# Kernel tuning notes

Measured on AMD Instinct MI355X. Metric: run time of the kernel, lower is better.

## Reference

```python
import jax, jax.numpy as jnp
import numpy as np

N_QUBITS = 6
N_LAYERS = 6
BATCH = 262144
DIM = 2 ** N_QUBITS  # 64 statevector amplitudes


def _apply_1q(s, U, q, n):
    # s: (M, 2^n) batch of statevectors, apply 2x2 gate U on wire q
    # (wire 0 = most significant bit, PennyLane convention)
    M = s.shape[0]
    st = s.reshape(M, 2 ** q, 2, 2 ** (n - 1 - q))
    out = jnp.einsum('ab,mxby->mxay', U, st)
    return out.reshape(M, 2 ** n)


def _apply_cnot(s, c, t, n):
    # CNOT(control=c, target=t): flip target bit where control bit == 1
    M = s.shape[0]
    a, b = (c, t) if c < t else (t, c)
    st = s.reshape(M, 2 ** a, 2, 2 ** (b - a - 1), 2, 2 ** (n - 1 - b))
    cax = 2 if c < t else 4
    tax = 4 if c < t else 2
    s0 = jnp.take(st, 0, axis=cax)
    s1 = jnp.take(st, 1, axis=cax)
    s1 = jnp.flip(s1, axis=tax - (1 if tax > cax else 0))
    out = jnp.stack([s0, s1], axis=cax)
    return out.reshape(M, 2 ** n)


def _rot(phi, theta, omega):
    # PennyLane Rot(phi, theta, omega) = RZ(omega) RY(theta) RZ(phi)
    c = jnp.cos(theta / 2).astype(jnp.complex64)
    s = jnp.sin(theta / 2).astype(jnp.complex64)
    ep = jnp.exp(-0.5j * (phi + omega).astype(jnp.complex64))
    em = jnp.exp(-0.5j * (phi - omega).astype(jnp.complex64))
    return jnp.stack([
        jnp.stack([ep * c, -jnp.conj(em) * s]),
        jnp.stack([em * s, jnp.conj(ep) * c]),
    ])


def _build_unitary_T(weights, n):
    # Compose the (input-independent) StronglyEntanglingLayers unitary G.
    # Rows of the result are G @ e_i, i.e. we return G^T, so psi_out = psi_in @ G^T.
    L = weights.shape[0]
    U = jnp.eye(2 ** n, dtype=jnp.complex64)
    for l in range(L):
        for j in range(n):
            U = _apply_1q(U, _rot(weights[l, j, 0], weights[l, j, 1], weights[l, j, 2]), j, n)
        r = (l % (n - 1)) + 1  # PennyLane default ranges
        for j in range(n):
            U = _apply_cnot(U, j, (j + r) % n, n)
    return U


def _forward(x, weights):
    B, n = x.shape
    # RY(pi*x_j)|0> = [cos(pi*x_j/2), sin(pi*x_j/2)] -> product state
    ang = (0.5 * jnp.pi) * x
    amps = jnp.stack([jnp.cos(ang), jnp.sin(ang)], axis=-1)  # (B, n, 2), real
    psi = amps[:, 0, :]
    for j in range(1, n):
        psi = (psi[:, :, None] * amps[:, j, None, :]).reshape(B, -1)
    # evolve by entangling unitary: (B, 64) @ (64, 64) complex GEMM
    psi = psi.astype(jnp.complex64) @ _build_unitary_T(weights, n)
    probs = psi.real ** 2 + psi.imag ** 2  # (B, 2^n)
    # <Z_k> = sum_i probs[i] * (+1 if bit_k(i)==0 else -1), wire 0 = MSB
    idx = np.arange(2 ** n)
    bits = (idx[:, None] >> (n - 1 - np.arange(n))) & 1
    signs = jnp.asarray(1.0 - 2.0 * bits, dtype=jnp.float32)  # (2^n, n)
    return probs @ signs  # (B, n) float32


def setup_inputs() -> dict:
    key = jax.random.key(0)
    k1, k2 = jax.random.split(key)
    x = jax.random.uniform(k1, (BATCH, N_QUBITS), dtype=jnp.float32)
    weights = jax.random.normal(k2, (N_LAYERS, N_QUBITS, 3), dtype=jnp.float32)
    return {"x": x, "weights": weights}


def reference(x, weights):
    return _forward(x, weights)
```

## Files before the change

### kernel.cpp

```cpp
#include <hip/hip_runtime.h>
#include <hip/hip_bf16.h>

#define NQ 6
#define DIM 64
#define NL 6

typedef _Float16 half8 __attribute__((ext_vector_type(8)));
typedef float f32x4 __attribute__((ext_vector_type(4)));

__global__ __launch_bounds__(256) void build_C_kernel(const float* __restrict__ w,
                                                      unsigned short* __restrict__ Cu) {
    __shared__ __align__(16) float Uc[NL * NQ][8];
    const int tid  = threadIdx.x;
    const int lane = tid & 63;
    const int wave = tid >> 6;
    const int col  = blockIdx.x * 4 + wave;

    if (tid < NL * NQ) {
        float phi = w[3 * tid], th = w[3 * tid + 1], om = w[3 * tid + 2];
        float ch = cosf(0.5f * th), sh = sinf(0.5f * th);
        float ap = -0.5f * (phi + om), am = -0.5f * (phi - om);
        float epr = cosf(ap), epi = sinf(ap);
        float emr = cosf(am), emi = sinf(am);
        Uc[tid][0] =  epr * ch;
        Uc[tid][1] =  epi * ch;
        Uc[tid][2] = -emr * sh;
        Uc[tid][3] =  emi * sh;
        Uc[tid][4] =  emr * sh;
        Uc[tid][5] =  emi * sh;
        Uc[tid][6] =  epr * ch;
        Uc[tid][7] = -epi * ch;
    }
    __syncthreads();

    float re = (lane == col) ? 1.f : 0.f;
    float im = 0.f;

    #pragma unroll
    for (int l = 0; l < NL; ++l) {
        #pragma unroll
        for (int j = 0; j < NQ; ++j) {
            const int g = l * NQ + j;
            const int m = 1 << (5 - j);
            float4 uA = *(const float4*)&Uc[g][0];
            float4 uB = *(const float4*)&Uc[g][4];
            float pr = __shfl_xor(re, m);
            float pi = __shfl_xor(im, m);
            const bool hi = (lane & m) != 0;
            float Ar = hi ? uB.z : uA.x;
            float Ai = hi ? uB.w : uA.y;
            float Br = hi ? uB.x : uA.z;
            float Bi = hi ? uB.y : uA.w;
            float nr = Ar * re - Ai * im + Br * pr - Bi * pi;
            float ni = Ar * im + Ai * re + Br * pi + Bi * pr;
            re = nr; im = ni;
        }
        const int r = l % (NQ - 1) + 1;
        int src = lane;
        #pragma unroll
        for (int jj = NQ - 1; jj >= 0; --jj) {
            int cm = 1 << (5 - jj);
            int tm = 1 << (5 - ((jj + r) % NQ));
            src = (src & cm) ? (src ^ tm) : src;
        }
        re = __shfl(re, src);
        im = __shfl(im, src);
    }

    _Float16 hr = (_Float16)re, hi16 = (_Float16)im;
    Cu[lane * 64 + col]        = __builtin_bit_cast(unsigned short, hr);
    Cu[4096 + lane * 64 + col] = __builtin_bit_cast(unsigned short, hi16);
}

__global__ __launch_bounds__(256) void qexp_mfma(const float* __restrict__ x,
                                                 const unsigned* __restrict__ C,
                                                 float* __restrict__ out,
                                                 int batch) {
    __shared__ __align__(16) unsigned Psi[256 * 36];
    const int tid  = threadIdx.x;
    const int lane = tid & 63;
    const int wave = tid >> 6;
    const int n    = lane & 15;
    const int g    = lane >> 4;
    const int sbase = blockIdx.x * 256 + wave * 64;

    half8 Ar[4][2], Ai[4][2];
    #pragma unroll
    for (int t = 0; t < 4; ++t)
        #pragma unroll
        for (int s = 0; s < 2; ++s) {
            int dw = (t * 16 + n) * 32 + s * 16 + g * 4;
            Ar[t][s] = __builtin_bit_cast(half8, *(const int4*)(C + dw));
            Ai[t][s] = __builtin_bit_cast(half8, *(const int4*)(C + 2048 + dw));
        }

    {
        const float2* xp = (const float2*)(x + (size_t)(sbase + lane) * NQ);
        float2 x01 = xp[0], x23 = xp[1], x45 = xp[2];
        float xa[6] = {x01.x, x01.y, x23.x, x23.y, x45.x, x45.y};
        float cs[6], sn[6];
        #pragma unroll
        for (int j = 0; j < 6; ++j) {
            float a = 1.57079632679489662f * xa[j];
            __sincosf(a, &sn[j], &cs[j]);
        }
        float a00 = cs[0] * cs[1], a01 = cs[0] * sn[1];
        float a10 = sn[0] * cs[1], a11 = sn[0] * sn[1];
        float hi[8] = {a00 * cs[2], a00 * sn[2], a01 * cs[2], a01 * sn[2],
                       a10 * cs[2], a10 * sn[2], a11 * cs[2], a11 * sn[2]};
        float b00 = cs[3] * cs[4], b01 = cs[3] * sn[4];
        float b10 = sn[3] * cs[4], b11 = sn[3] * sn[4];
        float lo[8] = {b00 * cs[5], b00 * sn[5], b01 * cs[5], b01 * sn[5],
                       b10 * cs[5], b10 * sn[5], b11 * cs[5], b11 * sn[5]};
        const int rowbase = tid * 36;
        #pragma unroll
        for (int c = 0; c < 8; ++c) {
            float h = hi[c];
            int4 d;
            d.x = __builtin_bit_cast(int, __builtin_amdgcn_cvt_pkrtz(h * lo[0], h * lo[1]));
            d.y = __builtin_bit_cast(int, __builtin_amdgcn_cvt_pkrtz(h * lo[2], h * lo[3]));
            d.z = __builtin_bit_cast(int, __builtin_amdgcn_cvt_pkrtz(h * lo[4], h * lo[5]));
            d.w = __builtin_bit_cast(int, __builtin_amdgcn_cvt_pkrtz(h * lo[6], h * lo[7]));
            *(int4*)(&Psi[rowbase + c * 4]) = d;
        }
    }
    __syncthreads();

    const unsigned m2 = (unsigned)(g >> 1) << 31;
    const unsigned m3 = (unsigned)(g & 1) << 31;

    #pragma unroll 1
    for (int grp = 0; grp < 4; ++grp) {
        f32x4 accr[4], acci[4];
        #pragma unroll
        for (int t = 0; t < 4; ++t) { accr[t] = (f32x4)0.f; acci[t] = (f32x4)0.f; }

        #pragma unroll
        for (int s = 0; s < 2; ++s) {
            int bd = (wave * 64 + grp * 16 + n) * 36 + s * 16 + g * 4;
            half8 B = __builtin_bit_cast(half8, *(const int4*)(&Psi[bd]));
            #pragma unroll
            for (int t = 0; t < 4; ++t) {
                accr[t] = __builtin_amdgcn_mfma_f32_16x16x32_f16(Ar[t][s], B, accr[t], 0, 0, 0);
                acci[t] = __builtin_amdgcn_mfma_f32_16x16x32_f16(Ai[t][s], B, acci[t], 0, 0, 0);
            }
        }

        float s01[4], s23[4], a02[4], T[4];
        #pragma unroll
        for (int t = 0; t < 4; ++t) {
            float p0 = fmaf(accr[t][0], accr[t][0], acci[t][0] * acci[t][0]);
            float p1 = fmaf(accr[t][1], accr[t][1], acci[t][1] * acci[t][1]);
            float p2 = fmaf(accr[t][2], accr[t][2], acci[t][2] * acci[t][2]);
            float p3 = fmaf(accr[t][3], accr[t][3], acci[t][3] * acci[t][3]);
            s01[t] = p0 + p1;
            s23[t] = p2 + p3;
            a02[t] = p0 + p2;
            T[t]   = s01[t] + s23[t];
        }
        float u = T[0] + T[1], v = T[2] + T[3];
        float P = u + v;
        float o0 = u - v;
        float w = T[0] + T[2];
        float o1 = fmaf(2.f, w, -P);
        float S01 = (s01[0] + s01[1]) + (s01[2] + s01[3]);
        float o4 = fmaf(2.f, S01, -P);
        float Sa = (a02[0] + a02[1]) + (a02[2] + a02[3]);
        float o5 = fmaf(2.f, Sa, -P);
        float o2 = __builtin_bit_cast(float, __builtin_bit_cast(unsigned, P) ^ m2);
        float o3 = __builtin_bit_cast(float, __builtin_bit_cast(unsigned, P) ^ m3);

        o0 += __shfl_xor(o0, 16); o0 += __shfl_xor(o0, 32);
        o1 += __shfl_xor(o1, 16); o1 += __shfl_xor(o1, 32);
        o2 += __shfl_xor(o2, 16); o2 += __shfl_xor(o2, 32);
        o3 += __shfl_xor(o3, 16); o3 += __shfl_xor(o3, 32);
        o4 += __shfl_xor(o4, 16); o4 += __shfl_xor(o4, 32);
        o5 += __shfl_xor(o5, 16); o5 += __shfl_xor(o5, 32);

        int sample = sbase + grp * 16 + n;
        float2* op = (float2*)(out + (size_t)sample * 6);
        if (g == 0)      { op[0] = make_float2(o0, o1); op[1] = make_float2(o2, o3); }
        else if (g == 1) { op[2] = make_float2(o4, o5); }
    }
}

extern "C" void kernel_launch(void* const* d_in, const int* in_sizes, int n_in,
                              void* d_out, int out_size, void* d_ws, size_t ws_size,
                              hipStream_t stream) {
    const float* x = (const float*)d_in[0];
    const float* w = (const float*)d_in[1];
    unsigned* C = (unsigned*)d_ws;
    float* out = (float*)d_out;
    const int batch = in_sizes[0] / NQ;

    build_C_kernel<<<16, 256, 0, stream>>>(w, (unsigned short*)C);
    const int blocks = (batch + 255) / 256;
    qexp_mfma<<<blocks, 256, 0, stream>>>(x, C, out, batch);
}
```

Baseline: 21.21 us.

## Build MFMA B operands directly in registers, dropping LDS staging and barrier

Each lane now computes its own product-state fragment for the MFMA B operand in registers, inside the per-group loop, instead of writing the full 64-amplitude state to shared memory and reading it back after a block barrier. This removes the LDS traffic, the 36KB shared allocation and the __syncthreads, and adds a launch-bounds occupancy hint. In exchange every lane recomputes the sincos terms for each of the 4 sample groups, so transcendental and ALU work is repeated 4 times per lane.

Result: slower. 24.12 us (+13.7%).

```diff
diff --git a/kernel.cpp b/kernel.cpp
--- a/kernel.cpp
+++ b/kernel.cpp
@@ -72,11 +72,10 @@
     Cu[4096 + lane * 64 + col] = __builtin_bit_cast(unsigned short, hi16);
 }
 
-__global__ __launch_bounds__(256) void qexp_mfma(const float* __restrict__ x,
-                                                 const unsigned* __restrict__ C,
-                                                 float* __restrict__ out,
-                                                 int batch) {
-    __shared__ __align__(16) unsigned Psi[256 * 36];
+__global__ __launch_bounds__(256, 4) void qexp_mfma(const float* __restrict__ x,
+                                                    const unsigned* __restrict__ C,
+                                                    float* __restrict__ out,
+                                                    int batch) {
     const int tid  = threadIdx.x;
     const int lane = tid & 63;
     const int wave = tid >> 6;
@@ -94,8 +93,14 @@
             Ai[t][s] = __builtin_bit_cast(half8, *(const int4*)(C + 2048 + dw));
         }
 
-    {
-        const float2* xp = (const float2*)(x + (size_t)(sbase + lane) * NQ);
+    const unsigned m2 = (unsigned)(g >> 1) << 31;
+    const unsigned m3 = (unsigned)(g & 1) << 31;
+
+    #pragma unroll 1
+    for (int grp = 0; grp < 4; ++grp) {
+        const int sample = sbase + grp * 16 + n;
+
+        const float2* xp = (const float2*)(x + (size_t)sample * NQ);
         float2 x01 = xp[0], x23 = xp[1], x45 = xp[2];
         float xa[6] = {x01.x, x01.y, x23.x, x23.y, x45.x, x45.y};
         float cs[6], sn[6];
@@ -104,65 +109,49 @@
             float a = 1.57079632679489662f * xa[j];
             __sincosf(a, &sn[j], &cs[j]);
         }
-        float a00 = cs[0] * cs[1], a01 = cs[0] * sn[1];
-        float a10 = sn[0] * cs[1], a11 = sn[0] * sn[1];
-        float hi[8] = {a00 * cs[2], a00 * sn[2], a01 * cs[2], a01 * sn[2],
-                       a10 * cs[2], a10 * sn[2], a11 * cs[2], a11 * sn[2]};
+
         float b00 = cs[3] * cs[4], b01 = cs[3] * sn[4];
         float b10 = sn[3] * cs[4], b11 = sn[3] * sn[4];
         float lo[8] = {b00 * cs[5], b00 * sn[5], b01 * cs[5], b01 * sn[5],
                        b10 * cs[5], b10 * sn[5], b11 * cs[5], b11 * sn[5]};
-        const int rowbase = tid * 36;
-        #pragma unroll
-        for (int c = 0; c < 8; ++c) {
-            float h = hi[c];
-            int4 d;
-            d.x = __builtin_bit_cast(int, __builtin_amdgcn_cvt_pkrtz(h * lo[0], h * lo[1]));
-            d.y = __builtin_bit_cast(int, __builtin_amdgcn_cvt_pkrtz(h * lo[2], h * lo[3]));
-            d.z = __builtin_bit_cast(int, __builtin_amdgcn_cvt_pkrtz(h * lo[4], h * lo[5]));
-            d.w = __builtin_bit_cast(int, __builtin_amdgcn_cvt_pkrtz(h * lo[6], h * lo[7]));
-            *(int4*)(&Psi[rowbase + c * 4]) = d;
-        }
-    }
-    __syncthreads();
+        float fg = ((g & 2) ? sn[1] : cs[1]) * ((g & 1) ? sn[2] : cs[2]);
+        float F0 = cs[0] * fg, F1 = sn[0] * fg;
 
-    const unsigned m2 = (unsigned)(g >> 1) << 31;
-    const unsigned m3 = (unsigned)(g & 1) << 31;
-
-    #pragma unroll 1
-    for (int grp = 0; grp < 4; ++grp) {
-        f32x4 accr[4], acci[4];
-        #pragma unroll
-        for (int t = 0; t < 4; ++t) { accr[t] = (f32x4)0.f; acci[t] = (f32x4)0.f; }
-
-        #pragma unroll
-        for (int s = 0; s < 2; ++s) {
-            int bd = (wave * 64 + grp * 16 + n) * 36 + s * 16 + g * 4;
-            half8 B = __builtin_bit_cast(half8, *(const int4*)(&Psi[bd]));
-            #pragma unroll
-            for (int t = 0; t < 4; ++t) {
-                accr[t] = __builtin_amdgcn_mfma_f32_16x16x32_f16(Ar[t][s], B, accr[t], 0, 0, 0);
-                acci[t] = __builtin_amdgcn_mfma_f32_16x16x32_f16(Ai[t][s], B, acci[t], 0, 0, 0);
-            }
-        }
+        int4 B0d, B1d;
+        B0d.x = __builtin_bit_cast(int, __builtin_amdgcn_cvt_pkrtz(F0 * lo[0], F0 * lo[1]));
+        B0d.y = __builtin_bit_cast(int, __builtin_amdgcn_cvt_pkrtz(F0 * lo[2], F0 * lo[3]));
+        B0d.z = __builtin_bit_cast(int, __builtin_amdgcn_cvt_pkrtz(F0 * lo[4], F0 * lo[5]));
+        B0d.w = __builtin_bit_cast(int, __builtin_amdgcn_cvt_pkrtz(F0 * lo[6], F0 * lo[7]));
+        B1d.x = __builtin_bit_cast(int, __builtin_amdgcn_cvt_pkrtz(F1 * lo[0], F1 * lo[1]));
+        B1d.y = __builtin_bit_cast(int, __builtin_amdgcn_cvt_pkrtz(F1 * lo[2], F1 * lo[3]));
+        B1d.z = __builtin_bit_cast(int, __builtin_amdgcn_cvt_pkrtz(F1 * lo[4], F1 * lo[5]));
+        B1d.w = __builtin_bit_cast(int, __builtin_amdgcn_cvt_pkrtz(F1 * lo[6], F1 * lo[7]));
+        half8 B0 = __builtin_bit_cast(half8, B0d);
+        half8 B1 = __builtin_bit_cast(half8, B1d);
 
         float s01[4], s23[4], a02[4], T[4];
         #pragma unroll
         for (int t = 0; t < 4; ++t) {
-            float p0 = fmaf(accr[t][0], accr[t][0], acci[t][0] * acci[t][0]);
-            float p1 = fmaf(accr[t][1], accr[t][1], acci[t][1] * acci[t][1]);
-            float p2 = fmaf(accr[t][2], accr[t][2], acci[t][2] * acci[t][2]);
-            float p3 = fmaf(accr[t][3], accr[t][3], acci[t][3] * acci[t][3]);
+            f32x4 ar = (f32x4)0.f, ai = (f32x4)0.f;
+            ar = __builtin_amdgcn_mfma_f32_16x16x32_f16(Ar[t][0], B0, ar, 0, 0, 0);
+            ar = __builtin_amdgcn_mfma_f32_16x16x32_f16(Ar[t][1], B1, ar, 0, 0, 0);
+            ai = __builtin_amdgcn_mfma_f32_16x16x32_f16(Ai[t][0], B0, ai, 0, 0, 0);
+            ai = __builtin_amdgcn_mfma_f32_16x16x32_f16(Ai[t][1], B1, ai, 0, 0, 0);
+            float p0 = fmaf(ar[0], ar[0], ai[0] * ai[0]);
+            float p1 = fmaf(ar[1], ar[1], ai[1] * ai[1]);
+            float p2 = fmaf(ar[2], ar[2], ai[2] * ai[2]);
+            float p3 = fmaf(ar[3], ar[3], ai[3] * ai[3]);
             s01[t] = p0 + p1;
             s23[t] = p2 + p3;
             a02[t] = p0 + p2;
             T[t]   = s01[t] + s23[t];
         }
+
         float u = T[0] + T[1], v = T[2] + T[3];
         float P = u + v;
         float o0 = u - v;
-        float w = T[0] + T[2];
-        float o1 = fmaf(2.f, w, -P);
+        float w2 = T[0] + T[2];
+        float o1 = fmaf(2.f, w2, -P);
         float S01 = (s01[0] + s01[1]) + (s01[2] + s01[3]);
         float o4 = fmaf(2.f, S01, -P);
         float Sa = (a02[0] + a02[1]) + (a02[2] + a02[3]);
@@ -177,7 +166,6 @@
         o4 += __shfl_xor(o4, 16); o4 += __shfl_xor(o4, 32);
         o5 += __shfl_xor(o5, 16); o5 += __shfl_xor(o5, 32);
 
-        int sample = sbase + grp * 16 + n;
         float2* op = (float2*)(out + (size_t)sample * 6);
         if (g == 0)      { op[0] = make_float2(o0, o1); op[1] = make_float2(o2, o3); }
         else if (g == 1) { op[2] = make_float2(o4, o5); }
```
